# Performance work log

Hardware: AMD Instinct MI355X
Metric: run time of the kernel (lower is better)

Reference implementation:

```python
import jax, jax.numpy as jnp
import numpy as np

N, S, E, H = 2, 2048, 1024, 16
D = E // H  # head dim = 64


def setup_inputs() -> dict:
    key = jax.random.key(0)
    ks = jax.random.split(key, 9)
    queries = jax.random.normal(ks[0], (N, S, E), dtype=jnp.float32)
    keys = jax.random.normal(ks[1], (N, S, E), dtype=jnp.float32)
    values = jax.random.normal(ks[2], (N, S, E), dtype=jnp.float32)
    mask = jax.random.randint(ks[3], (N, H, S, S), 0, 2, dtype=jnp.int32)
    # torch nn.Linear weights: shape (out_features, in_features), y = x @ W.T
    sc = 1.0 / np.sqrt(E)
    Wq = jax.random.uniform(ks[4], (E, E), jnp.float32, -sc, sc)
    Wk = jax.random.uniform(ks[5], (E, E), jnp.float32, -sc, sc)
    Wv = jax.random.uniform(ks[6], (E, E), jnp.float32, -sc, sc)
    Wo = jax.random.uniform(ks[7], (E, E), jnp.float32, -sc, sc)
    bo = jax.random.uniform(ks[8], (E,), jnp.float32, -sc, sc)
    return {"queries": queries, "keys": keys, "values": values, "mask": mask,
            "Wq": Wq, "Wk": Wk, "Wv": Wv, "Wo": Wo, "bo": bo}


def reference(queries, keys, values, mask, Wq, Wk, Wv, Wo, bo):
    n, d_q, _ = queries.shape
    d_k = keys.shape[1]
    q = (queries @ Wq.T).reshape(n, d_q, H, D)
    k = (keys @ Wk.T).reshape(n, d_k, H, D)
    v = (values @ Wv.T).reshape(n, d_k, H, D)
    energy = jnp.einsum('nqhd,nkhd->nhqk', q, k)
    energy = jnp.where(mask == 0, jnp.float32(-1e20), energy)
    # NOTE: module scales by sqrt of KEY SEQUENCE LENGTH, not head dim
    attn = jax.nn.softmax(energy / (d_k ** 0.5), axis=3)
    out = jnp.einsum('nhql,nlhd->nqhd', attn, v).reshape(n, d_q, E)
    return out @ Wo.T + bo
```

## Files before the change

### kernel.cpp

```cpp
#include <hip/hip_runtime.h>
#include <hip/hip_bf16.h>

#define DEVI __device__ __forceinline__

typedef __bf16 bf16x8 __attribute__((ext_vector_type(8)));
typedef float f32x4 __attribute__((ext_vector_type(4)));
typedef unsigned short u16x8 __attribute__((ext_vector_type(8)));
typedef unsigned short u16x4 __attribute__((ext_vector_type(4)));

constexpr int Nn = 2, Ss = 2048, Ee = 1024, Hh = 16;
constexpr int Ms = Nn * Ss;
constexpr float SCALE = 0.022097086912079608f;

constexpr size_t SZ_X   = (size_t)Ms * Ee;
constexpr size_t OFF_QB = 0;
constexpr size_t OFF_KB = SZ_X;
constexpr size_t OFF_VB = 2 * SZ_X;
constexpr size_t OFF_XQ = 3 * SZ_X;
constexpr size_t OFF_W  = 6 * SZ_X;
constexpr size_t OFF_ATTN = OFF_XQ;

DEVI unsigned short f2bf(float f) {
  unsigned int u = __builtin_bit_cast(unsigned int, f);
  u += 0x7fffu + ((u >> 16) & 1u);
  return (unsigned short)(u >> 16);
}

DEVI void async16(const void* g, void* l) {
  __builtin_amdgcn_global_load_lds(
      (const __attribute__((address_space(1))) void*)g,
      (__attribute__((address_space(3))) void*)l, 16, 0, 0);
}

DEVI f32x4 mfma_bf16(bf16x8 a, bf16x8 b, f32x4 c) {
  return __builtin_amdgcn_mfma_f32_16x16x32_bf16(a, b, c, 0, 0, 0);
}

__global__ __launch_bounds__(256) void cvt_batch(
    const float* __restrict__ s0, const float* __restrict__ s1,
    const float* __restrict__ s2, const float* __restrict__ s3,
    unsigned short* __restrict__ dbase, size_t dstride, int n4)
{
  const float* s = (blockIdx.z == 0) ? s0 : (blockIdx.z == 1) ? s1
                 : (blockIdx.z == 2) ? s2 : s3;
  unsigned short* d = dbase + (size_t)blockIdx.z * dstride;
  const int i = blockIdx.x * 256 + threadIdx.x;
  if (i >= n4) return;
  const float4 v = reinterpret_cast<const float4*>(s)[i];
  u16x4 o = { f2bf(v.x), f2bf(v.y), f2bf(v.z), f2bf(v.w) };
  reinterpret_cast<u16x4*>(d)[i] = o;
}

template <bool WRITE_F32>
__global__ __launch_bounds__(256) void gemm_bt(
    const unsigned short* __restrict__ Abase,
    const unsigned short* __restrict__ Bbase,
    unsigned short* __restrict__ Cbase,
    float* __restrict__ Cf,
    const float* __restrict__ bias,
    size_t strideA, size_t strideB, size_t strideC, int ldC)
{
  constexpr int K = 1024;
  __shared__ unsigned short As[128 * 32];
  __shared__ unsigned short Bs[128 * 32];

  const int z = blockIdx.z;
  const unsigned short* A = Abase + (size_t)z * strideA;
  const unsigned short* B = Bbase + (size_t)z * strideB;

  const int tid = threadIdx.x;
  const int lane = tid & 63, w = tid >> 6;
  const int lr = lane & 15, lg = lane >> 4;
  const int m0 = blockIdx.y * 128, n0 = blockIdx.x * 128;
  const int wr = (w >> 1) * 64, wc = (w & 1) * 64;

  const f32x4 zero = {0.f, 0.f, 0.f, 0.f};
  f32x4 acc[4][4];
  for (int a = 0; a < 4; ++a)
    for (int b = 0; b < 4; ++b) acc[a][b] = zero;

  for (int k0 = 0; k0 < K; k0 += 32) {
#pragma unroll
    for (int ii = 0; ii < 2; ++ii) {
      const int i = 2 * w + ii;
      const int boff = i * 1024 + lane * 16;
      const int row = boff >> 6;
      const int colb = boff & 63;
      const char* ga = (const char*)A + ((size_t)(m0 + row) * K + k0) * 2 + colb;
      const char* gb = (const char*)B + ((size_t)(n0 + row) * K + k0) * 2 + colb;
      async16(ga, (char*)As + i * 1024);
      async16(gb, (char*)Bs + i * 1024);
    }
    __syncthreads();

    bf16x8 aF[4], bF[4];
#pragma unroll
    for (int rb = 0; rb < 4; ++rb)
      aF[rb] = *(const bf16x8*)(As + (wr + rb * 16 + lr) * 32 + lg * 8);
#pragma unroll
    for (int cb = 0; cb < 4; ++cb)
      bF[cb] = *(const bf16x8*)(Bs + (wc + cb * 16 + lr) * 32 + lg * 8);
#pragma unroll
    for (int rb = 0; rb < 4; ++rb)
#pragma unroll
      for (int cb = 0; cb < 4; ++cb)
        acc[rb][cb] = mfma_bf16(aF[rb], bF[cb], acc[rb][cb]);
    __syncthreads();
  }

#pragma unroll
  for (int rb = 0; rb < 4; ++rb) {
#pragma unroll
    for (int cb = 0; cb < 4; ++cb) {
#pragma unroll
      for (int j = 0; j < 4; ++j) {
        const int row = m0 + wr + rb * 16 + lg * 4 + j;
        const int col = n0 + wc + cb * 16 + lr;
        const float v = acc[rb][cb][j];
        if constexpr (WRITE_F32) {
          Cf[(size_t)row * ldC + col] = v + bias[col];
        } else {
          unsigned short* C = Cbase + (size_t)z * strideC;
          C[(size_t)row * ldC + col] = f2bf(v);
        }
      }
    }
  }
}

__global__ __launch_bounds__(256) void attn_kernel(
    const unsigned short* __restrict__ Qb,
    const unsigned short* __restrict__ Kb,
    const unsigned short* __restrict__ Vtb,
    const int* __restrict__ mask,
    unsigned short* __restrict__ Ob)
{
  __shared__ unsigned short Kl0[64 * 64], Kl1[64 * 64];
  __shared__ unsigned short Vl0[64 * 64], Vl1[64 * 64];
  __shared__ unsigned short Pl[64 * 72];

  const int tid = threadIdx.x;
  const int lane = tid & 63, w = tid >> 6;
  const int lr = lane & 15, lg = lane >> 4;

  const int lid = blockIdx.x;
  const int xcd = lid & 7, slot = lid >> 3;
  const int g = xcd + 8 * (slot >> 5);
  const int n = g >> 4, h = g & 15;
  const int q0 = (slot & 31) * 64;

  bf16x8 aQ[2];
  {
    const unsigned short* qp =
        Qb + ((size_t)(n * Ss + q0 + w * 16 + lr)) * Ee + h * 64 + lg * 8;
    aQ[0] = *(const bf16x8*)(qp);
    aQ[1] = *(const bf16x8*)(qp + 32);
  }

  const int sig0 = (w * 2) * 64 + lane;
  const int row0 = sig0 >> 3;
  const int c0 = (sig0 & 7) ^ (row0 & 7);
  const int row1 = row0 + 8;
  const int c1 = (sig0 & 7) ^ (row1 & 7);
  const int ldsb0 = (w * 2 + 0) * 1024;
  const int ldsb1 = (w * 2 + 1) * 1024;

  const unsigned short* kp0 = Kb + ((size_t)(n * Ss + row0) * Ee + h * 64 + c0 * 8);
  const unsigned short* kp1 = Kb + ((size_t)(n * Ss + row1) * Ee + h * 64 + c1 * 8);
  const unsigned short* vp0 = Vtb + ((size_t)(h * 64 + row0) * Ms + n * Ss + c0 * 8);
  const unsigned short* vp1 = Vtb + ((size_t)(h * 64 + row1) * Ms + n * Ss + c1 * 8);

  const int* mp = mask + ((size_t)(n * Hh + h)) * Ss * Ss
                       + (size_t)(q0 + w * 16 + lg * 4) * Ss + lr;

  const f32x4 zero = {0.f, 0.f, 0.f, 0.f};
  f32x4 oacc[4] = {zero, zero, zero, zero};
  float rs[4] = {0.f, 0.f, 0.f, 0.f};

  async16(kp0, (char*)Kl0 + ldsb0);
  async16(kp1, (char*)Kl0 + ldsb1);
  async16(vp0, (char*)Vl0 + ldsb0);
  async16(vp1, (char*)Vl0 + ldsb1);
  kp0 += (size_t)64 * Ee; kp1 += (size_t)64 * Ee; vp0 += 64; vp1 += 64;

  int mv[4][4], mvN[4][4];
#pragma unroll
  for (int cb = 0; cb < 4; ++cb)
#pragma unroll
    for (int j = 0; j < 4; ++j)
      mv[cb][j] = __builtin_nontemporal_load(mp + (size_t)j * Ss + cb * 16);

  __syncthreads();

  int cur = 0;
  for (int kt = 0; kt < Ss / 64; ++kt) {
    const unsigned short* Kc = cur ? Kl1 : Kl0;
    const unsigned short* Vc = cur ? Vl1 : Vl0;
    unsigned short* Kn = cur ? Kl0 : Kl1;
    unsigned short* Vn = cur ? Vl0 : Vl1;

    if (kt + 1 < Ss / 64) {
      async16(kp0, (char*)Kn + ldsb0);
      async16(kp1, (char*)Kn + ldsb1);
      async16(vp0, (char*)Vn + ldsb0);
      async16(vp1, (char*)Vn + ldsb1);
      kp0 += (size_t)64 * Ee; kp1 += (size_t)64 * Ee; vp0 += 64; vp1 += 64;
#pragma unroll
      for (int cb = 0; cb < 4; ++cb)
#pragma unroll
        for (int j = 0; j < 4; ++j)
          mvN[cb][j] = __builtin_nontemporal_load(
              mp + (size_t)(kt + 1) * 64 + (size_t)j * Ss + cb * 16);
    }

    f32x4 s4[4];
    __builtin_amdgcn_s_setprio(1);
#pragma unroll
    for (int cb = 0; cb < 4; ++cb) {
      f32x4 a = zero;
#pragma unroll
      for (int kc = 0; kc < 2; ++kc) {
        const int row = cb * 16 + lr;
        bf16x8 bF = *(const bf16x8*)((const char*)Kc + row * 128 +
                                     (((kc * 4 + lg) ^ (row & 7)) * 16));
        a = mfma_bf16(aQ[kc], bF, a);
      }
      s4[cb] = a;
    }
    __builtin_amdgcn_s_setprio(0);

#pragma unroll
    for (int cb = 0; cb < 4; ++cb)
#pragma unroll
      for (int j = 0; j < 4; ++j) {
        const int qr = w * 16 + lg * 4 + j;
        const int kk = cb * 16 + lr;
        float p = mv[cb][j] ? __expf(s4[cb][j] * SCALE) : 0.f;
        rs[j] += p;
        Pl[qr * 72 + kk] = f2bf(p);
      }

    bf16x8 aP[2];
    aP[0] = *(const bf16x8*)(Pl + (w * 16 + lr) * 72 + lg * 8);
    aP[1] = *(const bf16x8*)(Pl + (w * 16 + lr) * 72 + 32 + lg * 8);
    __builtin_amdgcn_s_setprio(1);
#pragma unroll
    for (int db = 0; db < 4; ++db)
#pragma unroll
      for (int kc = 0; kc < 2; ++kc) {
        const int row = db * 16 + lr;
        bf16x8 bV = *(const bf16x8*)((const char*)Vc + row * 128 +
                                     (((kc * 4 + lg) ^ (row & 7)) * 16));
        oacc[db] = mfma_bf16(aP[kc], bV, oacc[db]);
      }
    __builtin_amdgcn_s_setprio(0);

    __syncthreads();
#pragma unroll
    for (int cb = 0; cb < 4; ++cb)
#pragma unroll
      for (int j = 0; j < 4; ++j) mv[cb][j] = mvN[cb][j];
    cur ^= 1;
  }

#pragma unroll
  for (int j = 0; j < 4; ++j) {
    float r = rs[j];
#pragma unroll
    for (int m = 1; m < 16; m <<= 1) r += __shfl_xor(r, m, 64);
    rs[j] = 1.0f / r;
  }
#pragma unroll
  for (int db = 0; db < 4; ++db)
#pragma unroll
    for (int j = 0; j < 4; ++j) {
      const int qr = q0 + w * 16 + lg * 4 + j;
      Ob[((size_t)(n * Ss + qr)) * Ee + h * 64 + db * 16 + lr] =
          f2bf(oacc[db][j] * rs[j]);
    }
}

extern "C" void kernel_launch(void* const* d_in, const int* in_sizes, int n_in,
                              void* d_out, int out_size, void* d_ws, size_t ws_size,
                              hipStream_t stream) {
  const float* qin = (const float*)d_in[0];
  const float* kin = (const float*)d_in[1];
  const float* vin = (const float*)d_in[2];
  const int*   msk = (const int*)d_in[3];
  const float* Wq  = (const float*)d_in[4];
  const float* Wk  = (const float*)d_in[5];
  const float* Wv  = (const float*)d_in[6];
  const float* Wo  = (const float*)d_in[7];
  const float* bo  = (const float*)d_in[8];
  unsigned short* ws = (unsigned short*)d_ws;
  const size_t EE = (size_t)Ee * Ee;

  cvt_batch<<<dim3((unsigned)(SZ_X / 4 / 256), 1, 3), 256, 0, stream>>>(
      qin, kin, vin, nullptr, ws + OFF_XQ, SZ_X, (int)(SZ_X / 4));
  cvt_batch<<<dim3((unsigned)(EE / 4 / 256), 1, 4), 256, 0, stream>>>(
      Wq, Wk, Wv, Wo, ws + OFF_W, EE, (int)(EE / 4));

  gemm_bt<false><<<dim3(8, 32, 2), 256, 0, stream>>>(
      ws + OFF_XQ, ws + OFF_W, ws + OFF_QB, nullptr, nullptr,
      SZ_X, EE, SZ_X, Ee);

  gemm_bt<false><<<dim3(32, 8, 1), 256, 0, stream>>>(
      ws + OFF_W + 2 * EE, ws + OFF_XQ + 2 * SZ_X, ws + OFF_VB, nullptr, nullptr,
      0, 0, 0, Ms);

  attn_kernel<<<dim3(1024), 256, 0, stream>>>(
      ws + OFF_QB, ws + OFF_KB, ws + OFF_VB, msk, ws + OFF_ATTN);

  gemm_bt<true><<<dim3(8, 32, 1), 256, 0, stream>>>(
      ws + OFF_ATTN, ws + OFF_W + 3 * EE, nullptr,
      (float*)d_out, bo, 0, 0, 0, Ee);
}
```

Baseline: 247.5 us.

## Pre-pack int32 attention mask into bitmasks before the attention kernel

Adds a streaming kernel that reads the int32 mask once and packs it into 64-bit ballot bitmasks in workspace. The attention kernel then loads one 64-bit word per query row per key tile instead of sixteen int32 mask values per thread, decoding bits in registers. The aim is to take the large mask stream out of the compute-heavy attention loop so that loop is no longer bandwidth-bound. In exchange it adds a kernel launch, a serial dependency between the two kernels, and a small extra write and read of the packed mask, while the full int32 mask still has to be read.

Result: slower. 271.5 us (+9.7%).

```diff
diff --git a/kernel.cpp b/kernel.cpp
--- a/kernel.cpp
+++ b/kernel.cpp
@@ -7,6 +7,7 @@
 typedef float f32x4 __attribute__((ext_vector_type(4)));
 typedef unsigned short u16x8 __attribute__((ext_vector_type(8)));
 typedef unsigned short u16x4 __attribute__((ext_vector_type(4)));
+typedef unsigned long long ull;
 
 constexpr int Nn = 2, Ss = 2048, Ee = 1024, Hh = 16;
 constexpr int Ms = Nn * Ss;
@@ -18,6 +19,7 @@
 constexpr size_t OFF_VB = 2 * SZ_X;
 constexpr size_t OFF_XQ = 3 * SZ_X;
 constexpr size_t OFF_W  = 6 * SZ_X;
+constexpr size_t OFF_PACK = 6 * SZ_X + 4 * (size_t)Ee * Ee;
 constexpr size_t OFF_ATTN = OFF_XQ;
 
 DEVI unsigned short f2bf(float f) {
@@ -51,6 +53,29 @@
   reinterpret_cast<u16x4*>(d)[i] = o;
 }
 
+__global__ __launch_bounds__(256) void pack_mask(
+    const int* __restrict__ mask, ull* __restrict__ P64)
+{
+  const int lane = threadIdx.x & 63;
+  const int gw = (int)((blockIdx.x * 256 + threadIdx.x) >> 6);
+  for (int r = 0; r < 64; ++r) {
+    const size_t rgi = (size_t)r * 8192 + gw;
+    const int* mp = mask + rgi * 256 + lane;
+    const int m0 = __builtin_nontemporal_load(mp);
+    const int m1 = __builtin_nontemporal_load(mp + 64);
+    const int m2 = __builtin_nontemporal_load(mp + 128);
+    const int m3 = __builtin_nontemporal_load(mp + 192);
+    const ull b0 = __ballot(m0 != 0);
+    const ull b1 = __ballot(m1 != 0);
+    const ull b2 = __ballot(m2 != 0);
+    const ull b3 = __ballot(m3 != 0);
+    if (lane < 4) {
+      const ull v = lane == 0 ? b0 : lane == 1 ? b1 : lane == 2 ? b2 : b3;
+      P64[rgi * 4 + lane] = v;
+    }
+  }
+}
+
 template <bool WRITE_F32>
 __global__ __launch_bounds__(256) void gemm_bt(
     const unsigned short* __restrict__ Abase,
@@ -132,7 +157,7 @@
     const unsigned short* __restrict__ Qb,
     const unsigned short* __restrict__ Kb,
     const unsigned short* __restrict__ Vtb,
-    const int* __restrict__ mask,
+    const ull* __restrict__ P64,
     unsigned short* __restrict__ Ob)
 {
   __shared__ unsigned short Kl0[64 * 64], Kl1[64 * 64];
@@ -170,8 +195,7 @@
   const unsigned short* vp0 = Vtb + ((size_t)(h * 64 + row0) * Ms + n * Ss + c0 * 8);
   const unsigned short* vp1 = Vtb + ((size_t)(h * 64 + row1) * Ms + n * Ss + c1 * 8);
 
-  const int* mp = mask + ((size_t)(n * Hh + h)) * Ss * Ss
-                       + (size_t)(q0 + w * 16 + lg * 4) * Ss + lr;
+  const ull* mp = P64 + ((size_t)(n * Hh + h) * Ss + (q0 + w * 16 + lg * 4)) * 32;
 
   const f32x4 zero = {0.f, 0.f, 0.f, 0.f};
   f32x4 oacc[4] = {zero, zero, zero, zero};
@@ -183,12 +207,10 @@
   async16(vp1, (char*)Vl0 + ldsb1);
   kp0 += (size_t)64 * Ee; kp1 += (size_t)64 * Ee; vp0 += 64; vp1 += 64;
 
-  int mv[4][4], mvN[4][4];
-#pragma unroll
-  for (int cb = 0; cb < 4; ++cb)
-#pragma unroll
-    for (int j = 0; j < 4; ++j)
-      mv[cb][j] = __builtin_nontemporal_load(mp + (size_t)j * Ss + cb * 16);
+  uint2 mw[4], mwN[4];
+#pragma unroll
+  for (int j = 0; j < 4; ++j)
+    mw[j] = *(const uint2*)(mp + (size_t)j * 32);
 
   __syncthreads();
 
@@ -206,11 +228,8 @@
       async16(vp1, (char*)Vn + ldsb1);
       kp0 += (size_t)64 * Ee; kp1 += (size_t)64 * Ee; vp0 += 64; vp1 += 64;
 #pragma unroll
-      for (int cb = 0; cb < 4; ++cb)
-#pragma unroll
-        for (int j = 0; j < 4; ++j)
-          mvN[cb][j] = __builtin_nontemporal_load(
-              mp + (size_t)(kt + 1) * 64 + (size_t)j * Ss + cb * 16);
+      for (int j = 0; j < 4; ++j)
+        mwN[j] = *(const uint2*)(mp + (size_t)j * 32 + (kt + 1));
     }
 
     f32x4 s4[4];
@@ -235,7 +254,9 @@
       for (int j = 0; j < 4; ++j) {
         const int qr = w * 16 + lg * 4 + j;
         const int kk = cb * 16 + lr;
-        float p = mv[cb][j] ? __expf(s4[cb][j] * SCALE) : 0.f;
+        const unsigned word = (cb & 2) ? mw[j].y : mw[j].x;
+        const unsigned bit = (word >> ((cb & 1) * 16 + lr)) & 1u;
+        float p = bit ? __expf(s4[cb][j] * SCALE) : 0.f;
         rs[j] += p;
         Pl[qr * 72 + kk] = f2bf(p);
       }
@@ -257,9 +278,7 @@
 
     __syncthreads();
 #pragma unroll
-    for (int cb = 0; cb < 4; ++cb)
-#pragma unroll
-      for (int j = 0; j < 4; ++j) mv[cb][j] = mvN[cb][j];
+    for (int j = 0; j < 4; ++j) mw[j] = mwN[j];
     cur ^= 1;
   }
 
@@ -293,6 +312,7 @@
   const float* Wo  = (const float*)d_in[7];
   const float* bo  = (const float*)d_in[8];
   unsigned short* ws = (unsigned short*)d_ws;
+  ull* P64 = (ull*)(ws + OFF_PACK);
   const size_t EE = (size_t)Ee * Ee;
 
   cvt_batch<<<dim3((unsigned)(SZ_X / 4 / 256), 1, 3), 256, 0, stream>>>(
@@ -308,8 +328,10 @@
       ws + OFF_W + 2 * EE, ws + OFF_XQ + 2 * SZ_X, ws + OFF_VB, nullptr, nullptr,
       0, 0, 0, Ms);
 
+  pack_mask<<<dim3(2048), 256, 0, stream>>>(msk, P64);
+
   attn_kernel<<<dim3(1024), 256, 0, stream>>>(
-      ws + OFF_QB, ws + OFF_KB, ws + OFF_VB, msk, ws + OFF_ATTN);
+      ws + OFF_QB, ws + OFF_KB, ws + OFF_VB, P64, ws + OFF_ATTN);
 
   gemm_bt<true><<<dim3(8, 32, 1), 256, 0, stream>>>(
       ws + OFF_ATTN, ws + OFF_W + 3 * EE, nullptr,
```

## Double per-block query tile to 128 rows and reuse K/V loads

Applied to the files above, without the earlier changes.

Each attention block now processes 128 query rows (32 per wave) instead of 64, so every K/V tile staged in LDS feeds twice as many MFMAs, and the grid is halved to 512 blocks. Mask values are packed into a bitmask, and the next tile's mask is prefetched into the same registers, dropping the separate mvN copy. The end-of-iteration __syncthreads is replaced by a vmcnt wait plus barrier at the top of the loop. The goal is to halve K/V global and LDS traffic per query, at the cost of more registers, lower occupancy and fewer blocks to spread across CUs.

New measurement: 242.0 us. 2.2% less time.

```diff
diff --git a/kernel.cpp b/kernel.cpp
--- a/kernel.cpp
+++ b/kernel.cpp
@@ -7,6 +7,7 @@
 typedef float f32x4 __attribute__((ext_vector_type(4)));
 typedef unsigned short u16x8 __attribute__((ext_vector_type(8)));
 typedef unsigned short u16x4 __attribute__((ext_vector_type(4)));
+typedef unsigned long long ull;
 
 constexpr int Nn = 2, Ss = 2048, Ee = 1024, Hh = 16;
 constexpr int Ms = Nn * Ss;
@@ -137,7 +138,7 @@
 {
   __shared__ unsigned short Kl0[64 * 64], Kl1[64 * 64];
   __shared__ unsigned short Vl0[64 * 64], Vl1[64 * 64];
-  __shared__ unsigned short Pl[64 * 72];
+  __shared__ unsigned short Pl[128 * 72];
 
   const int tid = threadIdx.x;
   const int lane = tid & 63, w = tid >> 6;
@@ -145,16 +146,17 @@
 
   const int lid = blockIdx.x;
   const int xcd = lid & 7, slot = lid >> 3;
-  const int g = xcd + 8 * (slot >> 5);
+  const int g = xcd + 8 * (slot >> 4);
   const int n = g >> 4, h = g & 15;
-  const int q0 = (slot & 31) * 64;
-
-  bf16x8 aQ[2];
-  {
+  const int q0 = (slot & 15) * 128;
+
+  bf16x8 aQ[2][2];
+#pragma unroll
+  for (int qb = 0; qb < 2; ++qb) {
     const unsigned short* qp =
-        Qb + ((size_t)(n * Ss + q0 + w * 16 + lr)) * Ee + h * 64 + lg * 8;
-    aQ[0] = *(const bf16x8*)(qp);
-    aQ[1] = *(const bf16x8*)(qp + 32);
+        Qb + ((size_t)(n * Ss + q0 + w * 32 + qb * 16 + lr)) * Ee + h * 64 + lg * 8;
+    aQ[qb][0] = *(const bf16x8*)(qp);
+    aQ[qb][1] = *(const bf16x8*)(qp + 32);
   }
 
   const int sig0 = (w * 2) * 64 + lane;
@@ -171,11 +173,15 @@
   const unsigned short* vp1 = Vtb + ((size_t)(h * 64 + row1) * Ms + n * Ss + c1 * 8);
 
   const int* mp = mask + ((size_t)(n * Hh + h)) * Ss * Ss
-                       + (size_t)(q0 + w * 16 + lg * 4) * Ss + lr;
+                       + (size_t)(q0 + w * 32 + lg * 4) * Ss + lr;
 
   const f32x4 zero = {0.f, 0.f, 0.f, 0.f};
-  f32x4 oacc[4] = {zero, zero, zero, zero};
-  float rs[4] = {0.f, 0.f, 0.f, 0.f};
+  f32x4 oacc[2][4];
+#pragma unroll
+  for (int qb = 0; qb < 2; ++qb)
+#pragma unroll
+    for (int db = 0; db < 4; ++db) oacc[qb][db] = zero;
+  float rs[2][4] = {{0.f, 0.f, 0.f, 0.f}, {0.f, 0.f, 0.f, 0.f}};
 
   async16(kp0, (char*)Kl0 + ldsb0);
   async16(kp1, (char*)Kl0 + ldsb1);
@@ -183,21 +189,34 @@
   async16(vp1, (char*)Vl0 + ldsb1);
   kp0 += (size_t)64 * Ee; kp1 += (size_t)64 * Ee; vp0 += 64; vp1 += 64;
 
-  int mv[4][4], mvN[4][4];
-#pragma unroll
-  for (int cb = 0; cb < 4; ++cb)
+  int mv[2][4][4];
+#pragma unroll
+  for (int qb = 0; qb < 2; ++qb)
 #pragma unroll
     for (int j = 0; j < 4; ++j)
-      mv[cb][j] = __builtin_nontemporal_load(mp + (size_t)j * Ss + cb * 16);
-
-  __syncthreads();
+#pragma unroll
+      for (int cb = 0; cb < 4; ++cb)
+        mv[qb][j][cb] = __builtin_nontemporal_load(
+            mp + (size_t)(qb * 16 + j) * Ss + cb * 16);
 
   int cur = 0;
   for (int kt = 0; kt < Ss / 64; ++kt) {
+    asm volatile("s_waitcnt vmcnt(0)" ::: "memory");
+    __builtin_amdgcn_s_barrier();
+
     const unsigned short* Kc = cur ? Kl1 : Kl0;
     const unsigned short* Vc = cur ? Vl1 : Vl0;
     unsigned short* Kn = cur ? Kl0 : Kl1;
     unsigned short* Vn = cur ? Vl0 : Vl1;
+
+    unsigned mbits = 0;
+#pragma unroll
+    for (int qb = 0; qb < 2; ++qb)
+#pragma unroll
+      for (int j = 0; j < 4; ++j)
+#pragma unroll
+        for (int cb = 0; cb < 4; ++cb)
+          mbits |= (mv[qb][j][cb] != 0 ? 1u : 0u) << (((qb * 4 + j) * 4) + cb);
 
     if (kt + 1 < Ss / 64) {
       async16(kp0, (char*)Kn + ldsb0);
@@ -206,78 +225,89 @@
       async16(vp1, (char*)Vn + ldsb1);
       kp0 += (size_t)64 * Ee; kp1 += (size_t)64 * Ee; vp0 += 64; vp1 += 64;
 #pragma unroll
+      for (int qb = 0; qb < 2; ++qb)
+#pragma unroll
+        for (int j = 0; j < 4; ++j)
+#pragma unroll
+          for (int cb = 0; cb < 4; ++cb)
+            mv[qb][j][cb] = __builtin_nontemporal_load(
+                mp + (size_t)(qb * 16 + j) * Ss + (size_t)(kt + 1) * 64 + cb * 16);
+    }
+
+#pragma unroll
+    for (int qb = 0; qb < 2; ++qb) {
+      f32x4 s4[4];
+      __builtin_amdgcn_s_setprio(1);
+#pragma unroll
+      for (int cb = 0; cb < 4; ++cb) {
+        f32x4 a = zero;
+#pragma unroll
+        for (int kc = 0; kc < 2; ++kc) {
+          const int row = cb * 16 + lr;
+          bf16x8 bF = *(const bf16x8*)((const char*)Kc + row * 128 +
+                                       (((kc * 4 + lg) ^ (row & 7)) * 16));
+          a = mfma_bf16(aQ[qb][kc], bF, a);
+        }
+        s4[cb] = a;
+      }
+      __builtin_amdgcn_s_setprio(0);
+
+#pragma unroll
       for (int cb = 0; cb < 4; ++cb)
 #pragma unroll
-        for (int j = 0; j < 4; ++j)
-          mvN[cb][j] = __builtin_nontemporal_load(
-              mp + (size_t)(kt + 1) * 64 + (size_t)j * Ss + cb * 16);
-    }
-
-    f32x4 s4[4];
+        for (int j = 0; j < 4; ++j) {
+          const int qr = w * 32 + qb * 16 + lg * 4 + j;
+          const int kk = cb * 16 + lr;
+          const unsigned bit = (mbits >> (((qb * 4 + j) * 4) + cb)) & 1u;
+          float p = bit ? __expf(s4[cb][j] * SCALE) : 0.f;
+          rs[qb][j] += p;
+          Pl[qr * 72 + kk] = f2bf(p);
+        }
+    }
+
+    bf16x8 aP[2][2];
+#pragma unroll
+    for (int qb = 0; qb < 2; ++qb) {
+      aP[qb][0] = *(const bf16x8*)(Pl + (w * 32 + qb * 16 + lr) * 72 + lg * 8);
+      aP[qb][1] = *(const bf16x8*)(Pl + (w * 32 + qb * 16 + lr) * 72 + 32 + lg * 8);
+    }
     __builtin_amdgcn_s_setprio(1);
 #pragma unroll
-    for (int cb = 0; cb < 4; ++cb) {
-      f32x4 a = zero;
+    for (int db = 0; db < 4; ++db) {
+      const int row = db * 16 + lr;
 #pragma unroll
       for (int kc = 0; kc < 2; ++kc) {
-        const int row = cb * 16 + lr;
-        bf16x8 bF = *(const bf16x8*)((const char*)Kc + row * 128 +
-                                     (((kc * 4 + lg) ^ (row & 7)) * 16));
-        a = mfma_bf16(aQ[kc], bF, a);
-      }
-      s4[cb] = a;
-    }
-    __builtin_amdgcn_s_setprio(0);
-
-#pragma unroll
-    for (int cb = 0; cb < 4; ++cb)
-#pragma unroll
-      for (int j = 0; j < 4; ++j) {
-        const int qr = w * 16 + lg * 4 + j;
-        const int kk = cb * 16 + lr;
-        float p = mv[cb][j] ? __expf(s4[cb][j] * SCALE) : 0.f;
-        rs[j] += p;
-        Pl[qr * 72 + kk] = f2bf(p);
-      }
-
-    bf16x8 aP[2];
-    aP[0] = *(const bf16x8*)(Pl + (w * 16 + lr) * 72 + lg * 8);
-    aP[1] = *(const bf16x8*)(Pl + (w * 16 + lr) * 72 + 32 + lg * 8);
-    __builtin_amdgcn_s_setprio(1);
-#pragma unroll
-    for (int db = 0; db < 4; ++db)
-#pragma unroll
-      for (int kc = 0; kc < 2; ++kc) {
-        const int row = db * 16 + lr;
         bf16x8 bV = *(const bf16x8*)((const char*)Vc + row * 128 +
                                      (((kc * 4 + lg) ^ (row & 7)) * 16));
-        oacc[db] = mfma_bf16(aP[kc], bV, oacc[db]);
+#pragma unroll
+        for (int qb = 0; qb < 2; ++qb)
+          oacc[qb][db] = mfma_bf16(aP[qb][kc], bV, oacc[qb][db]);
       }
+    }
     __builtin_amdgcn_s_setprio(0);
 
-    __syncthreads();
-#pragma unroll
-    for (int cb = 0; cb < 4; ++cb)
-#pragma unroll
-      for (int j = 0; j < 4; ++j) mv[cb][j] = mvN[cb][j];
     cur ^= 1;
   }
 
 #pragma unroll
-  for (int j = 0; j < 4; ++j) {
-    float r = rs[j];
-#pragma unroll
-    for (int m = 1; m < 16; m <<= 1) r += __shfl_xor(r, m, 64);
-    rs[j] = 1.0f / r;
-  }
-#pragma unroll
-  for (int db = 0; db < 4; ++db)
+  for (int qb = 0; qb < 2; ++qb)
 #pragma unroll
     for (int j = 0; j < 4; ++j) {
-      const int qr = q0 + w * 16 + lg * 4 + j;
-      Ob[((size_t)(n * Ss + qr)) * Ee + h * 64 + db * 16 + lr] =
-          f2bf(oacc[db][j] * rs[j]);
-    }
+      float r = rs[qb][j];
+#pragma unroll
+      for (int m = 1; m < 16; m <<= 1) r += __shfl_xor(r, m, 64);
+      rs[qb][j] = 1.0f / r;
+    }
+#pragma unroll
+  for (int qb = 0; qb < 2; ++qb)
+#pragma unroll
+    for (int db = 0; db < 4; ++db)
+#pragma unroll
+      for (int j = 0; j < 4; ++j) {
+        const int qr = q0 + w * 32 + qb * 16 + lg * 4 + j;
+        Ob[((size_t)(n * Ss + qr)) * Ee + h * 64 + db * 16 + lr] =
+            f2bf(oacc[qb][db][j] * rs[qb][j]);
+      }
 }
 
 extern "C" void kernel_launch(void* const* d_in, const int* in_sizes, int n_in,
@@ -308,7 +338,7 @@
       ws + OFF_W + 2 * EE, ws + OFF_XQ + 2 * SZ_X, ws + OFF_VB, nullptr, nullptr,
       0, 0, 0, Ms);
 
-  attn_kernel<<<dim3(1024), 256, 0, stream>>>(
+  attn_kernel<<<dim3(512), 256, 0, stream>>>(
       ws + OFF_QB, ws + OFF_KB, ws + OFF_VB, msk, ws + OFF_ATTN);
 
   gemm_bt<true><<<dim3(8, 32, 1), 256, 0, stream>>>(
```
